# Performance work log

Measured on AMD Instinct MI355X. Metric: run time of the kernel, lower is better.

The kernel has to match this reference:

```python
import jax, jax.numpy as jnp
import numpy as np

BN_EPS = 1e-5

def conv1x1(x, w, b):
    # x: [N,C,T,V], w: [O,C], b: [O]
    return jnp.einsum('nctv,oc->notv', x, w) + b[None, :, None, None]

def conv9(x, w, b):
    # (9,1) temporal conv, padding (4,0). x: [N,C,T,V], w: [O,C,9], b: [O]
    out = jax.lax.conv_general_dilated(
        x, w[:, :, :, None], window_strides=(1, 1), padding=((4, 4), (0, 0)),
        dimension_numbers=('NCHW', 'OIHW', 'NCHW'))
    return out + b[None, :, None, None]

def attn_adj(f1, f2):
    # f1,f2: [N,inter,T,V] -> softmax over rows (axis -2) of [N,V,V]
    N, ic, T, V = f1.shape
    a1 = jnp.transpose(f1, (0, 3, 1, 2)).reshape(N, V, ic * T)  # permute(0,3,1,2).view
    a2 = f2.reshape(N, ic * T, V)
    scores = jnp.einsum('nvk,nkw->nvw', a1, a2) / (ic * T)
    return jax.nn.softmax(scores, axis=-2)


def setup_inputs() -> dict:
    key = jax.random.key(0)
    ks = jax.random.split(key, 16)
    N, C, T, V, S, IC = 16, 256, 64, 25, 3, 64
    s = lambda k, shape, sc=0.05: jax.random.normal(k, shape, dtype=jnp.float32) * sc
    return {
        'x': jax.random.normal(ks[0], (N, C, T, V), dtype=jnp.float32),
        'A': jax.random.uniform(ks[1], (S, V, V), dtype=jnp.float32),
        'PA': s(ks[2], (S, V, V), 1e-3),
        'wa': s(ks[3], (S, IC, C)), 'ba': jnp.zeros((S, IC), jnp.float32),
        'wb': s(ks[4], (S, IC, C)), 'bb': jnp.zeros((S, IC), jnp.float32),
        'wT1': s(ks[5], (S, IC, C, 9)), 'bT1': jnp.zeros((S, IC), jnp.float32),
        'wT2': s(ks[6], (S, IC, C, 9)), 'bT2': jnp.zeros((S, IC), jnp.float32),
        'wST11': s(ks[7], (S, IC, C, 9)), 'bST11': jnp.zeros((S, IC), jnp.float32),
        'wST12': s(ks[8], (S, IC, C, 9)), 'bST12': jnp.zeros((S, IC), jnp.float32),
        'wd': s(ks[9], (S, C, C)), 'bd': jnp.zeros((S, C), jnp.float32),
        'gamma': jnp.ones((C,), jnp.float32), 'beta': jnp.zeros((C,), jnp.float32),
        'bn_mean': jnp.zeros((C,), jnp.float32), 'bn_var': jnp.ones((C,), jnp.float32),
    }


def reference(x, A, PA, wa, ba, wb, bb, wT1, bT1, wT2, bT2,
              wST11, bST11, wST12, bST12, wd, bd, gamma, beta, bn_mean, bn_var):
    N, C, T, V = x.shape
    I = jnp.eye(V, dtype=x.dtype)
    # Chebyshev-like static graph transforms (computed once in __init__ in torch)
    A_ch4s = jax.nn.softmax((8 * A**4 - 4 * A**2 - 4 * A + I) / V, axis=-2)
    A_ch3 = 4 * A**2 - A - 2 * I
    A_all = A_ch3 + A_ch4s + PA  # [3,V,V]

    xf = x.reshape(N, C * T, V)
    y = 0.0
    for i in range(3):
        A1 = attn_adj(conv1x1(x, wa[i], ba[i]), conv1x1(x, wb[i], bb[i]))
        AT = attn_adj(conv9(x, wT1[i], bT1[i]), conv9(x, wT2[i], bT2[i]))
        # ModuleList append quirk: even i -> 1x1 conv (center tap), odd i -> (9,1) conv
        if i % 2 == 0:
            s1 = conv1x1(x, wST11[i, :, :, 4], bST11[i])
            s2 = conv1x1(x, wST12[i, :, :, 4], bST12[i])
        else:
            s1 = conv9(x, wST11[i], bST11[i])
            s2 = conv9(x, wST12[i], bST12[i])
        AST = attn_adj(s1, s2)
        Ai = A_all[i] + A1 + AT + AST  # [N,V,V]
        z = jnp.einsum('nkv,nvw->nkw', xf, Ai).reshape(N, C, T, V)
        y = y + conv1x1(z, wd[i], bd[i])

    yb = (y - bn_mean[None, :, None, None]) * (gamma[None, :, None, None]
         / jnp.sqrt(bn_var[None, :, None, None] + BN_EPS)) + beta[None, :, None, None]
    return jax.nn.relu(yb + x)  # down is identity (in_channels == out_channels)
```

## Files before the change

### kernel.cpp

```cpp
#include <hip/hip_runtime.h>
#include <hip/hip_bf16.h>

#define NN 16
#define CC 256
#define TT 64
#define VV 25
#define ICC 64
#define TV 1600
#define CTV 409600
#define NICTV 1638400

typedef __bf16 v8bf __attribute__((ext_vector_type(8)));
typedef __bf16 v4bf __attribute__((ext_vector_type(4)));
typedef float f32x16 __attribute__((ext_vector_type(16)));

struct ConvPairs {
  const __bf16* wA[5];
  const __bf16* wB[5];
  const float*  bA[5];
  const float*  bB[5];
};

__device__ __forceinline__ void gl_lds16(const __bf16* g, __bf16* l){
  __builtin_amdgcn_global_load_lds(
      (const __attribute__((address_space(1))) unsigned int*)g,
      (__attribute__((address_space(3))) unsigned int*)l, 16, 0, 0);
}

__global__ __launch_bounds__(256) void prep_k(
    const float* __restrict__ x, __bf16* __restrict__ xt,
    const float* __restrict__ wT1, const float* __restrict__ wT2,
    const float* __restrict__ wST11, const float* __restrict__ wST12,
    __bf16* __restrict__ wT1p, __bf16* __restrict__ wT2p,
    __bf16* __restrict__ wS1p, __bf16* __restrict__ wS2p,
    const float* __restrict__ wa, const float* __restrict__ wb,
    __bf16* __restrict__ wabp, __bf16* __restrict__ wScp,
    const float* __restrict__ wd, __bf16* __restrict__ wdb,
    const float* __restrict__ A, const float* __restrict__ PA,
    float* __restrict__ Aall, __bf16* __restrict__ zp){
  __shared__ __align__(16) float smf[64*65];
  __bf16* smb = (__bf16*)smf;
  int b = blockIdx.x;
  int tid = threadIdx.x;
  if (b < 64){
    int t = b >> 3, ch64 = (b >> 1) & 3, o2 = b & 1;
    const float* src; __bf16* dst;
    if (t < 3)      { src = wT1  + (size_t)t*147456;     dst = wT1p + (size_t)t*147456; }
    else if (t < 6) { src = wT2  + (size_t)(t-3)*147456; dst = wT2p + (size_t)(t-3)*147456; }
    else if (t == 6){ src = wST11 + 147456;              dst = wS1p; }
    else            { src = wST12 + 147456;              dst = wS2p; }
    const float* in = src + (size_t)(o2*32)*2304 + ch64*576;
    for (int i = tid; i < 32*576; i += 256){
      int row = i / 576, cc = i % 576;
      smb[i] = (__bf16)in[(size_t)row*2304 + cc];
    }
    __syncthreads();
    for (int i = tid; i < 18432; i += 256){
      int e = i & 7, l = (i >> 3) & 63, ks = (i >> 9) & 1;
      int r10 = i >> 10;
      int tap = r10 % 9, chh = r10 / 9;
      int ol = l & 31, hh = l >> 5;
      int cl = ks*16 + hh*8 + e;
      int c64 = chh*32 + cl;
      int ch8 = ch64*2 + chh;
      dst[(size_t)((((ch8*9 + tap)*2 + ks)*2 + o2)*512) + l*8 + e]
          = smb[ol*576 + c64*9 + tap];
    }
  } else if (b < 74){
    int u = b - 64;
    for (int it = 0; it < 8; ++it){
      int i = tid + it*256;
      int e = i & 7, l = (i >> 3) & 63, o2 = (i >> 9) & 1;
      int ks = (i >> 10) & 1, ch = i >> 11;
      int ol = l & 31, hh = l >> 5;
      int o = o2*32 + ol;
      int c = ch*32 + ks*16 + hh*8 + e;
      __bf16 v;
      if (u < 6){
        const float* w = (u < 3) ? (wa + (size_t)u*16384) : (wb + (size_t)(u-3)*16384);
        v = (__bf16)w[(size_t)o*256 + c];
      } else {
        int i9 = ((u == 6) || (u == 8)) ? 0 : 2;
        const float* w = ((u < 8) ? wST11 : wST12) + (size_t)i9*147456;
        v = (__bf16)w[((size_t)o*256 + c)*9 + 4];
      }
      __bf16* dst = (u < 6) ? (wabp + (size_t)u*16384) : (wScp + (size_t)(u-6)*16384);
      dst[i] = v;
    }
  } else if (b < 842){
    int i = (b-74)*256 + tid;
    if (i < 196608) wdb[i] = (__bf16)wd[i];
  } else if (b == 842){
    int t = tid;
    if (t < 75){
      int s = t / 25, w = t % 25;
      float a[25], m[25];
      float mx = -3.4e38f;
      for (int v = 0; v < 25; ++v){
        float av = A[(s*25 + v)*25 + w];
        a[v] = av;
        float d = (v == w) ? 1.f : 0.f;
        float mm = (8.f*av*av*av*av - 4.f*av*av - 4.f*av + d) * 0.04f;
        m[v] = mm;
        mx = fmaxf(mx, mm);
      }
      float sum = 0.f;
      for (int v = 0; v < 25; ++v){ float e = __expf(m[v]-mx); m[v] = e; sum += e; }
      float inv = 1.f/sum;
      for (int v = 0; v < 25; ++v){
        float av = a[v];
        float d = (v == w) ? 1.f : 0.f;
        Aall[(s*25+v)*25 + w] = m[v]*inv + 4.f*av*av - av - 2.f*d + PA[(s*25+v)*25+w];
      }
    } else if (t >= 128){
      zp[t-128] = (__bf16)0.f;
    }
  } else {
    int idx = b - 843;
    int p0 = (idx % 25)*64, c0 = ((idx/25) & 3)*64, n = idx/100;
    for (int i = tid; i < 4096; i += 256){
      int cc = i >> 6, pp = i & 63;
      smf[cc*65+pp] = x[(size_t)n*CTV + (size_t)(c0+cc)*TV + p0 + pp];
    }
    __syncthreads();
    for (int i = tid; i < 4096; i += 256){
      int pp = i >> 6, cc = i & 63;
      xt[((size_t)n*TV + p0+pp)*256 + c0+cc] = (__bf16)smf[cc*65+pp];
    }
  }
}

template<int NTAPS, int MINW>
__global__ __launch_bounds__(512, MINW) void conv15_k(const __bf16* __restrict__ xt,
    ConvPairs cp, const __bf16* __restrict__ zp, __bf16* __restrict__ fbuf){
  extern __shared__ __bf16 sm[];
  constexpr int HALO  = (NTAPS==9) ? 100 : 0;
  constexpr int NROWS = 256 + 2*HALO;
  constexpr int SLOTS = NROWS*4;
  constexpr int KSTG  = (SLOTS + 511)/512;
  constexpr int NSTEP = NTAPS*2;
  constexpr int AELE  = NTAPS*2*2*512;
  constexpr int ASLT  = 2*AELE/8;
  constexpr int DEP   = (NSTEP >= 3) ? 3 : 2;
  int p0 = blockIdx.x*256;
  int n  = blockIdx.y;
  int pr = blockIdx.z;
  int tid = threadIdx.x;
  int lane = tid & 63;
  int wave = tid >> 6;
  int which = wave >> 2, wq = wave & 3;
  int h = lane >> 5, l31 = lane & 31;
  const __bf16* xtn = xt + (size_t)n*CTV;
  const __bf16* wg0 = cp.wA[pr];
  const __bf16* wg1 = cp.wB[pr];
  __bf16* xb0 = sm;
  __bf16* xb1 = sm + NROWS*32;
  __bf16* Ab  = sm + 2*NROWS*32;

  f32x16 acc[2][2];
  #pragma unroll
  for (int a=0;a<2;++a)
    #pragma unroll
    for (int b=0;b<2;++b)
      #pragma unroll
      for (int r=0;r<16;++r) acc[a][b][r] = 0.f;

  int rowbase = wq*64 + l31;

  auto stageX = [&](__bf16* bn, int ch){
    #pragma unroll
    for (int k=0; k<KSTG; ++k){
      int slot = k*512 + tid;
      if ((SLOTS & 511) && slot >= SLOTS) continue;
      const __bf16* src;
      if (NTAPS == 1){
        int l31s = slot & 31, f = slot >> 5;
        int h_ = f & 1, ks_ = (f >> 1) & 1, pblk = f >> 2;
        int pg = p0 + pblk*32 + l31s;
        src = (pg < 1600) ? (xtn + (size_t)pg*256 + ch*32 + ks_*16 + h_*8)
                          : zp;
      } else {
        int row = slot >> 2, g2 = slot & 3;
        int g = (g2 - (row>>1)) & 3;
        int pg = p0 - HALO + row;
        src = ((unsigned)pg < 1600u) ? (xtn + (size_t)pg*256 + ch*32 + g*8)
                                     : zp;
      }
      gl_lds16(src, bn + (size_t)slot*8);
    }
  };
  auto stageA = [&](int ch){
    #pragma unroll
    for (int k=0; k<(ASLT+511)/512; ++k){
      int slot = k*512 + tid;
      if ((ASLT & 511) && slot >= ASLT) continue;
      int cv = (slot >= AELE/8) ? 1 : 0;
      int off = (slot - cv*(AELE/8))*8;
      const __bf16* src = (cv ? wg1 : wg0) + (size_t)ch*AELE + off;
      gl_lds16(src, Ab + cv*AELE + off);
    }
  };
  const __bf16* aw = Ab + which*AELE + lane*8;
  auto ldA = [&](int s, v8bf* aa){
    int off = s*1024;
    aa[0] = *(const v8bf*)(aw + off);
    aa[1] = *(const v8bf*)(aw + off + 512);
  };
  auto ldB = [&](const __bf16* bc, int s, v8bf* bb){
    int tap = s >> 1, ks = s & 1;
    #pragma unroll
    for (int pq=0; pq<2; ++pq){
      if (NTAPS == 1){
        int frag = ((wq*2 + pq)*2 + ks)*2 + h;
        bb[pq] = *(const v8bf*)(bc + frag*256 + l31*8);
      } else {
        int row = tap*25 + rowbase + pq*32;
        int gs = ((ks*2 + h) + (row>>1)) & 3;
        bb[pq] = *(const v8bf*)(bc + row*32 + gs*8);
      }
    }
  };

  stageA(0);
  stageX(xb0, 0);
  __syncthreads();

  v8bf ar[DEP][2], bR[DEP][2];
  for (int ch=0; ch<8; ++ch){
    const __bf16* bc = (ch & 1) ? xb1 : xb0;
    __bf16*       bn = (ch & 1) ? xb0 : xb1;
    if (ch < 7) stageX(bn, ch+1);
    #pragma unroll
    for (int i=0; i<DEP; ++i){
      if (i < NSTEP){ ldA(i, ar[i]); ldB(bc, i, bR[i]); }
    }
    #pragma unroll
    for (int s=0; s<NSTEP; ++s){
      int c = s % DEP;
      v8bf A0 = ar[c][0], A1 = ar[c][1];
      v8bf B0 = bR[c][0], B1 = bR[c][1];
      if (s+DEP < NSTEP){
        ldB(bc, s+DEP, bR[c]);
        ldA(s+DEP, ar[c]);
      }
      __builtin_amdgcn_s_setprio(1);
      acc[0][0] = __builtin_amdgcn_mfma_f32_32x32x16_bf16(A0, B0, acc[0][0], 0,0,0);
      acc[1][0] = __builtin_amdgcn_mfma_f32_32x32x16_bf16(A1, B0, acc[1][0], 0,0,0);
      acc[0][1] = __builtin_amdgcn_mfma_f32_32x32x16_bf16(A0, B1, acc[0][1], 0,0,0);
      acc[1][1] = __builtin_amdgcn_mfma_f32_32x32x16_bf16(A1, B1, acc[1][1], 0,0,0);
      __builtin_amdgcn_s_setprio(0);
    }
    __syncthreads();
    if (ch < 7) stageA(ch+1);
    __syncthreads();
  }

  const float* bias = which ? cp.bB[pr] : cp.bA[pr];
  __bf16* outb = fbuf + (size_t)(pr*2 + which)*NICTV + (size_t)n*TV*64;
  #pragma unroll
  for (int pq=0; pq<2; ++pq){
    int p = p0 + wq*64 + pq*32 + l31;
    if (p >= 1600) continue;
    __bf16* orow = outb + (size_t)p*64;
    #pragma unroll
    for (int of=0; of<2; ++of){
      #pragma unroll
      for (int g=0; g<4; ++g){
        int og = of*32 + 8*g + 4*h;
        v4bf pk;
        #pragma unroll
        for (int j=0;j<4;++j) pk[j] = (__bf16)(acc[of][pq][4*g+j] + bias[og+j]);
        *(v4bf*)(orow + og) = pk;
      }
    }
  }
}

__global__ __launch_bounds__(256, 2) void ugemm6_k(const __bf16* __restrict__ xt,
    const __bf16* __restrict__ wdb, __bf16* __restrict__ ubuf){
  __shared__ __bf16 sm[64*256];
  int p0 = blockIdx.x*64;
  int n  = blockIdx.y;
  int tid = threadIdx.x;
  int lane = tid & 63;
  int os = tid >> 6;
  int h = lane >> 5, l31 = lane & 31;
  const __bf16* xtn = xt + (size_t)n*CTV;

  for (int s2 = tid; s2 < 64*32; s2 += 256){
    int row = s2 >> 5, g = s2 & 31;
    uint4 val = *(const uint4*)(xtn + (size_t)(p0+row)*256 + g*8);
    int gs = (g + row) & 31;
    *(uint4*)(sm + row*256 + gs*8) = val;
  }
  __syncthreads();

  auto ldB = [&](int ks, v8bf* bb){
    #pragma unroll
    for (int pq=0; pq<2; ++pq){
      int row = pq*32 + l31;
      int gs = ((ks*2 + h) + row) & 31;
      bb[pq] = *(const v8bf*)(sm + row*256 + gs*8);
    }
  };

  for (int br=0; br<3; ++br){
    const __bf16* wl = wdb + ((size_t)br*256 + os*64 + l31)*256 + h*8;
    auto ldA = [&](int ks, v8bf& A0, v8bf& A1){
      A0 = *(const v8bf*)(wl + ks*16);
      A1 = *(const v8bf*)(wl + (size_t)32*256 + ks*16);
    };
    f32x16 acc[2][2];
    #pragma unroll
    for (int a=0;a<2;++a)
      #pragma unroll
      for (int b=0;b<2;++b)
        #pragma unroll
        for (int r=0;r<16;++r) acc[a][b][r] = 0.f;

    v8bf a0[4], a1[4];
    ldA(0, a0[0], a1[0]);
    ldA(1, a0[1], a1[1]);
    ldA(2, a0[2], a1[2]);
    ldA(3, a0[3], a1[3]);
    v8bf bR[2][2];
    ldB(0, bR[0]);
    ldB(1, bR[1]);
    #pragma unroll
    for (int ks=0; ks<16; ++ks){
      int c2 = ks & 1, cur = ks & 3;
      v8bf B0 = bR[c2][0], B1 = bR[c2][1];
      v8bf A0 = a0[cur], A1 = a1[cur];
      if (ks+2 < 16) ldB(ks+2, bR[c2]);
      if (ks+4 < 16) ldA(ks+4, a0[cur], a1[cur]);
      acc[0][0] = __builtin_amdgcn_mfma_f32_32x32x16_bf16(A0, B0, acc[0][0], 0,0,0);
      acc[1][0] = __builtin_amdgcn_mfma_f32_32x32x16_bf16(A1, B0, acc[1][0], 0,0,0);
      acc[0][1] = __builtin_amdgcn_mfma_f32_32x32x16_bf16(A0, B1, acc[0][1], 0,0,0);
      acc[1][1] = __builtin_amdgcn_mfma_f32_32x32x16_bf16(A1, B1, acc[1][1], 0,0,0);
    }

    #pragma unroll
    for (int pq=0; pq<2; ++pq){
      int p = p0 + pq*32 + l31;
      __bf16* out = ubuf + ((size_t)(br*NN + n)*TV + p)*256;
      #pragma unroll
      for (int oq=0; oq<2; ++oq){
        #pragma unroll
        for (int g=0; g<4; ++g){
          int og = os*64 + oq*32 + 8*g + 4*h;
          v4bf pk;
          #pragma unroll
          for (int j=0;j<4;++j) pk[j] = (__bf16)acc[oq][pq][4*g+j];
          *(v4bf*)(out + og) = pk;
        }
      }
    }
  }
}

__global__ __launch_bounds__(256) void scores_m2_k(const __bf16* __restrict__ fbuf,
                                                   float* __restrict__ part, int pairbase){
  __shared__ float smp[4][1024];
  int bx = blockIdx.x, n = blockIdx.y, pr = blockIdx.z;
  int tid = threadIdx.x;
  int lane = tid & 63;
  int wave = tid >> 6;
  int chunk = bx*4 + wave;
  int h = lane >> 5, l31 = lane & 31;
  const __bf16* f1 = fbuf + (size_t)(pr*2)*NICTV   + (size_t)n*TV*64;
  const __bf16* f2 = fbuf + (size_t)(pr*2+1)*NICTV + (size_t)n*TV*64;
  int t0 = chunk*4;

  f32x16 acc;
  #pragma unroll
  for (int r=0;r<16;++r) acc[r] = 0.f;

  auto off = [&](int s)->size_t{
    int t = t0 + (s>>2), og = s&3;
    return ((size_t)(t*25 + l31))*64 + og*16 + h*8;
  };
  v8bf A[4], B[4];
  #pragma unroll
  for (int i=0; i<4; ++i){
    size_t o = off(i);
    A[i] = *(const v8bf*)(f1+o); B[i] = *(const v8bf*)(f2+o);
  }
  #pragma unroll
  for (int s=0; s<16; ++s){
    int cur = s & 3;
    v8bf Ac = A[cur], Bc = B[cur];
    if (s+4 < 16){
      size_t o2 = off(s+4);
      A[cur] = *(const v8bf*)(f1+o2);
      B[cur] = *(const v8bf*)(f2+o2);
    }
    acc = __builtin_amdgcn_mfma_f32_32x32x16_bf16(Ac, Bc, acc, 0,0,0);
  }

  #pragma unroll
  for (int r=0; r<16; ++r){
    int row = (r&3) + 8*(r>>2) + 4*h;
    smp[wave][row*32 + l31] = acc[r];
  }
  __syncthreads();
  for (int j = tid; j < 1024; j += 256){
    float s = smp[0][j] + smp[1][j] + smp[2][j] + smp[3][j];
    part[(((size_t)(pairbase+pr)*NN + n)*4 + bx)*1024 + j] = s;
  }
}

__global__ __launch_bounds__(800) void finalize2_k(const float* __restrict__ part,
    const float* __restrict__ Aall, float* __restrict__ Ai3){
  __shared__ float smR[25][33];
  int n = blockIdx.x, br = blockIdx.y;
  int w = threadIdx.x;
  int v = threadIdx.y;
  const int prs0[3] = {0,3,5}, prs1[3] = {1,6,8}, prs2[3] = {2,4,7};
  const int* prs = (br==0) ? prs0 : (br==1) ? prs1 : prs2;
  float acc = 0.f;
  for (int k=0; k<3; ++k){
    const float* pb = part + ((size_t)prs[k]*NN + n)*4096;
    float s = 0.f;
    if (w < 25){
      s = pb[v*32+w] + pb[1024+v*32+w] + pb[2048+v*32+w] + pb[3072+v*32+w];
      s *= (1.f/4096.f);
    }
    smR[v][w] = s;
    __syncthreads();
    #pragma unroll
    for (int d=16; d>0; d>>=1){
      if (v < d){
        float o = (v+d < 25) ? smR[v+d][w] : -3.4e38f;
        smR[v][w] = fmaxf(smR[v][w], o);
      }
      __syncthreads();
    }
    float mx = smR[0][w];
    __syncthreads();
    float e = __expf(s - mx);
    smR[v][w] = e;
    __syncthreads();
    #pragma unroll
    for (int d=16; d>0; d>>=1){
      if (v < d){
        float o = (v+d < 25) ? smR[v+d][w] : 0.f;
        smR[v][w] += o;
      }
      __syncthreads();
    }
    float sum = smR[0][w];
    __syncthreads();
    acc += e / sum;
  }
  if (w < 25)
    Ai3[((size_t)br*NN + n)*625 + v*25 + w] =
      Aall[br*625 + v*25 + w] + acc;
}

__global__ __launch_bounds__(256) void yep_k(const float* __restrict__ x,
    const float* __restrict__ Ai3, const __bf16* __restrict__ ubuf,
    const float* __restrict__ bd, const float* __restrict__ gamma,
    const float* __restrict__ beta, const float* __restrict__ bnm,
    const float* __restrict__ bnv, float* __restrict__ out){
  __shared__ float ais[3][25*28];
  __shared__ float xs[6400];
  int t = blockIdx.x, n = blockIdx.y, o = threadIdx.x;
  for (int l=o; l<2100; l+=256){
    int br = l/700, r = l%700;
    int v = r/28, w = r%28;
    ais[br][v*28+w] = (w<25) ? Ai3[((size_t)br*NN + n)*625 + v*25 + w] : 0.f;
  }
  for (int li=o; li<6400; li+=256){
    int oo = li/25, ww = li%25;
    xs[li] = x[(size_t)n*CTV + (size_t)oo*TV + t*25 + ww];
  }
  __syncthreads();
  float y[28];
  #pragma unroll
  for (int w=0;w<28;++w) y[w]=0.f;
  for (int br=0; br<3; ++br){
    const __bf16* up = ubuf + ((size_t)(br*NN + n)*TV + t*25)*256 + o;
    float uv[25];
    #pragma unroll
    for (int v=0;v<25;++v) uv[v] = (float)up[(size_t)v*256];
    const float* ab = ais[br];
    for (int v=0; v<25; ++v){
      float u = uv[v];
      #pragma unroll
      for (int j=0; j<7; ++j){
        float4 a4 = *(const float4*)(ab + v*28 + 4*j);
        y[4*j+0] = fmaf(u, a4.x, y[4*j+0]);
        y[4*j+1] = fmaf(u, a4.y, y[4*j+1]);
        y[4*j+2] = fmaf(u, a4.z, y[4*j+2]);
        y[4*j+3] = fmaf(u, a4.w, y[4*j+3]);
      }
    }
  }
  float bsum = bd[o] + bd[256+o] + bd[512+o];
  float sc = gamma[o] * rsqrtf(bnv[o] + 1e-5f);
  float m  = bnm[o], be = beta[o];
  #pragma unroll
  for (int w=0; w<25; ++w)
    xs[o*25+w] = fmaxf((y[w] + bsum - m)*sc + be + xs[o*25+w], 0.f);
  __syncthreads();
  for (int li=o; li<6400; li+=256){
    int oo = li/25, ww = li%25;
    out[(size_t)n*CTV + (size_t)oo*TV + t*25 + ww] = xs[li];
  }
}

extern "C" void kernel_launch(void* const* d_in, const int* in_sizes, int n_in,
                              void* d_out, int out_size, void* d_ws, size_t ws_size,
                              hipStream_t stream) {
  const float* x     = (const float*)d_in[0];
  const float* A     = (const float*)d_in[1];
  const float* PA    = (const float*)d_in[2];
  const float* wa    = (const float*)d_in[3];
  const float* ba    = (const float*)d_in[4];
  const float* wb    = (const float*)d_in[5];
  const float* bb    = (const float*)d_in[6];
  const float* wT1   = (const float*)d_in[7];
  const float* bT1   = (const float*)d_in[8];
  const float* wT2   = (const float*)d_in[9];
  const float* bT2   = (const float*)d_in[10];
  const float* wST11 = (const float*)d_in[11];
  const float* bST11 = (const float*)d_in[12];
  const float* wST12 = (const float*)d_in[13];
  const float* bST12 = (const float*)d_in[14];
  const float* wd    = (const float*)d_in[15];
  const float* bd    = (const float*)d_in[16];
  const float* gamma = (const float*)d_in[17];
  const float* beta  = (const float*)d_in[18];
  const float* bnm   = (const float*)d_in[19];
  const float* bnv   = (const float*)d_in[20];

  char* W = (char*)d_ws;
  float*  Aall = (float*)W;  W += 8192;
  __bf16* zp   = (__bf16*)W; W += 256;
  float*  Ai3  = (float*)W;  W += 122880;
  __bf16* wabp = (__bf16*)W; W += 196608;
  __bf16* wScp = (__bf16*)W; W += 131072;
  __bf16* wT1p = (__bf16*)W; W += 884736;
  __bf16* wT2p = (__bf16*)W; W += 884736;
  __bf16* wS1p = (__bf16*)W; W += 294912;
  __bf16* wS2p = (__bf16*)W; W += 294912;
  __bf16* wdb  = (__bf16*)W; W += 393216;
  __bf16* xt   = (__bf16*)W; W += 13107200;
  char* R = W;               W += 39321600;
  float*  part = (float*)W;  W += 2359296;
  __bf16* fbuf = (__bf16*)R;
  __bf16* ubuf = (__bf16*)R;

  prep_k<<<2443, 256, 0, stream>>>(x, xt, wT1, wT2, wST11, wST12,
                                   wT1p, wT2p, wS1p, wS2p,
                                   wa, wb, wabp, wScp, wd, wdb, A, PA, Aall, zp);

  {
    ConvPairs cp;
    for (int i=0;i<3;++i){
      cp.wA[i] = wabp + (size_t)i*16384;      cp.wB[i] = wabp + (size_t)(3+i)*16384;
      cp.bA[i] = ba + i*64;                   cp.bB[i] = bb + i*64;
    }
    int evens[2] = {0, 2};
    for (int j=0;j<2;++j){
      int i = evens[j];
      cp.wA[3+j] = wScp + (size_t)j*16384;    cp.wB[3+j] = wScp + (size_t)(2+j)*16384;
      cp.bA[3+j] = bST11 + i*64;              cp.bB[3+j] = bST12 + i*64;
    }
    conv15_k<1,4><<<dim3(7,16,5), 512, 40960, stream>>>(xt, cp, zp, fbuf);
    scores_m2_k<<<dim3(4,16,5), 256, 0, stream>>>(fbuf, part, 0);
  }

  {
    ConvPairs cp;
    for (int i=0;i<3;++i){
      cp.wA[i] = wT1p + (size_t)i*147456;  cp.wB[i] = wT2p + (size_t)i*147456;
      cp.bA[i] = bT1 + i*64;               cp.bB[i] = bT2 + i*64;
    }
    cp.wA[3] = wS1p;  cp.wB[3] = wS2p;
    cp.bA[3] = bST11 + 64;  cp.bB[3] = bST12 + 64;
    cp.wA[4] = cp.wA[3]; cp.wB[4] = cp.wB[3]; cp.bA[4] = cp.bA[3]; cp.bB[4] = cp.bB[3];
    conv15_k<9,2><<<dim3(7,16,4), 512, 132096, stream>>>(xt, cp, zp, fbuf);
    scores_m2_k<<<dim3(4,16,4), 256, 0, stream>>>(fbuf, part, 5);
  }

  ugemm6_k<<<dim3(25,16), 256, 0, stream>>>(xt, wdb, ubuf);
  finalize2_k<<<dim3(16,3), dim3(32,25), 0, stream>>>(part, Aall, Ai3);
  yep_k<<<dim3(64,16), 256, 0, stream>>>(x, Ai3, ubuf, bd, gamma, beta, bnm, bnv,
                                         (float*)d_out);
}
```

Before: 332.8 us.

## Process two timesteps per block in epilogue and read padded adjacency from global

The epilogue kernel now handles two consecutive timesteps per block, so each adjacency value loaded is reused for twice the FMAs and the grid is halved. The finalize kernel writes the adjacency already padded to 28 columns in an n-major layout, and the epilogue reads it straight from global memory instead of staging it through shared memory. In exchange, per-thread register use doubles (two 28-float accumulators and two 25-float input arrays), which puts pressure on occupancy, and shared memory per block rises to two x tiles.

```diff
diff --git a/kernel.cpp b/kernel.cpp
--- a/kernel.cpp
+++ b/kernel.cpp
@@ -409,8 +409,8 @@
   }
 }
 
-__global__ __launch_bounds__(800) void finalize2_k(const float* __restrict__ part,
-    const float* __restrict__ Aall, float* __restrict__ Ai3){
+__global__ __launch_bounds__(800) void finalize3_k(const float* __restrict__ part,
+    const float* __restrict__ Aall, float* __restrict__ aisg){
   __shared__ float smR[25][33];
   int n = blockIdx.x, br = blockIdx.y;
   int w = threadIdx.x;
@@ -452,47 +452,51 @@
     __syncthreads();
     acc += e / sum;
   }
-  if (w < 25)
-    Ai3[((size_t)br*NN + n)*625 + v*25 + w] =
-      Aall[br*625 + v*25 + w] + acc;
-}
-
-__global__ __launch_bounds__(256) void yep_k(const float* __restrict__ x,
-    const float* __restrict__ Ai3, const __bf16* __restrict__ ubuf,
+  if (w < 28){
+    float val = (w < 25) ? (Aall[br*625 + v*25 + w] + acc) : 0.f;
+    aisg[((size_t)n*3 + br)*700 + v*28 + w] = val;
+  }
+}
+
+__global__ __launch_bounds__(256, 2) void yep3_k(const float* __restrict__ x,
+    const float* __restrict__ aisg, const __bf16* __restrict__ ubuf,
     const float* __restrict__ bd, const float* __restrict__ gamma,
     const float* __restrict__ beta, const float* __restrict__ bnm,
     const float* __restrict__ bnv, float* __restrict__ out){
-  __shared__ float ais[3][25*28];
-  __shared__ float xs[6400];
-  int t = blockIdx.x, n = blockIdx.y, o = threadIdx.x;
-  for (int l=o; l<2100; l+=256){
-    int br = l/700, r = l%700;
-    int v = r/28, w = r%28;
-    ais[br][v*28+w] = (w<25) ? Ai3[((size_t)br*NN + n)*625 + v*25 + w] : 0.f;
-  }
-  for (int li=o; li<6400; li+=256){
-    int oo = li/25, ww = li%25;
-    xs[li] = x[(size_t)n*CTV + (size_t)oo*TV + t*25 + ww];
+  __shared__ float xs[2][6400];
+  int t2 = blockIdx.x, n = blockIdx.y, o = threadIdx.x;
+  int t0 = t2*2;
+  for (int li=o; li<12800; li+=256){
+    int dt = li / 6400, r = li % 6400;
+    int oo = r/25, ww = r%25;
+    xs[dt][r] = x[(size_t)n*CTV + (size_t)oo*TV + (t0+dt)*25 + ww];
   }
   __syncthreads();
-  float y[28];
-  #pragma unroll
-  for (int w=0;w<28;++w) y[w]=0.f;
+  float y0[28], y1[28];
+  #pragma unroll
+  for (int w=0;w<28;++w){ y0[w]=0.f; y1[w]=0.f; }
   for (int br=0; br<3; ++br){
-    const __bf16* up = ubuf + ((size_t)(br*NN + n)*TV + t*25)*256 + o;
-    float uv[25];
-    #pragma unroll
-    for (int v=0;v<25;++v) uv[v] = (float)up[(size_t)v*256];
-    const float* ab = ais[br];
+    const __bf16* up = ubuf + ((size_t)(br*NN + n)*TV + t0*25)*256 + o;
+    float u0[25], u1[25];
+    #pragma unroll
+    for (int v=0;v<25;++v){
+      u0[v] = (float)up[(size_t)v*256];
+      u1[v] = (float)up[(size_t)(v+25)*256];
+    }
+    const float* ab = aisg + ((size_t)n*3 + br)*700;
     for (int v=0; v<25; ++v){
-      float u = uv[v];
+      float a0 = u0[v], a1 = u1[v];
       #pragma unroll
       for (int j=0; j<7; ++j){
         float4 a4 = *(const float4*)(ab + v*28 + 4*j);
-        y[4*j+0] = fmaf(u, a4.x, y[4*j+0]);
-        y[4*j+1] = fmaf(u, a4.y, y[4*j+1]);
-        y[4*j+2] = fmaf(u, a4.z, y[4*j+2]);
-        y[4*j+3] = fmaf(u, a4.w, y[4*j+3]);
+        y0[4*j+0] = fmaf(a0, a4.x, y0[4*j+0]);
+        y0[4*j+1] = fmaf(a0, a4.y, y0[4*j+1]);
+        y0[4*j+2] = fmaf(a0, a4.z, y0[4*j+2]);
+        y0[4*j+3] = fmaf(a0, a4.w, y0[4*j+3]);
+        y1[4*j+0] = fmaf(a1, a4.x, y1[4*j+0]);
+        y1[4*j+1] = fmaf(a1, a4.y, y1[4*j+1]);
+        y1[4*j+2] = fmaf(a1, a4.z, y1[4*j+2]);
+        y1[4*j+3] = fmaf(a1, a4.w, y1[4*j+3]);
       }
     }
   }
@@ -500,12 +504,15 @@
   float sc = gamma[o] * rsqrtf(bnv[o] + 1e-5f);
   float m  = bnm[o], be = beta[o];
   #pragma unroll
-  for (int w=0; w<25; ++w)
-    xs[o*25+w] = fmaxf((y[w] + bsum - m)*sc + be + xs[o*25+w], 0.f);
+  for (int w=0; w<25; ++w){
+    xs[0][o*25+w] = fmaxf((y0[w] + bsum - m)*sc + be + xs[0][o*25+w], 0.f);
+    xs[1][o*25+w] = fmaxf((y1[w] + bsum - m)*sc + be + xs[1][o*25+w], 0.f);
+  }
   __syncthreads();
-  for (int li=o; li<6400; li+=256){
-    int oo = li/25, ww = li%25;
-    out[(size_t)n*CTV + (size_t)oo*TV + t*25 + ww] = xs[li];
+  for (int li=o; li<12800; li+=256){
+    int dt = li / 6400, r = li % 6400;
+    int oo = r/25, ww = r%25;
+    out[(size_t)n*CTV + (size_t)oo*TV + (t0+dt)*25 + ww] = xs[dt][r];
   }
 }
 
@@ -537,7 +544,7 @@
   char* W = (char*)d_ws;
   float*  Aall = (float*)W;  W += 8192;
   __bf16* zp   = (__bf16*)W; W += 256;
-  float*  Ai3  = (float*)W;  W += 122880;
+  float*  aisg = (float*)W;  W += 135168;
   __bf16* wabp = (__bf16*)W; W += 196608;
   __bf16* wScp = (__bf16*)W; W += 131072;
   __bf16* wT1p = (__bf16*)W; W += 884736;
@@ -585,7 +592,7 @@
   }
 
   ugemm6_k<<<dim3(25,16), 256, 0, stream>>>(xt, wdb, ubuf);
-  finalize2_k<<<dim3(16,3), dim3(32,25), 0, stream>>>(part, Aall, Ai3);
-  yep_k<<<dim3(64,16), 256, 0, stream>>>(x, Ai3, ubuf, bd, gamma, beta, bnm, bnv,
-                                         (float*)d_out);
-}
+  finalize3_k<<<dim3(16,3), dim3(32,25), 0, stream>>>(part, Aall, aisg);
+  yep3_k<<<dim3(32,16), 256, 0, stream>>>(x, aisg, ubuf, bd, gamma, beta, bnm, bnv,
+                                          (float*)d_out);
+}
```

Result: faster. 322.1 us (-3.2%).
